# Kernel tuning notes

Hardware: AMD Instinct MI355X
Metric: run time of the kernel (lower is better)

## Reference

```python
import jax, jax.numpy as jnp
import numpy as np

EPS = 1e-4
RMS_EPS = 1e-5

def _rms_norm(x, w):
    # RMSNorm over last dim
    var = jnp.mean(x * x, axis=-1, keepdims=True)
    return x * jax.lax.rsqrt(var + RMS_EPS) * w


def setup_inputs() -> dict:
    key = jax.random.key(0)
    ks = jax.random.split(key, 6)
    T, d, h = 8192, 2048, 8192
    x = jax.random.normal(ks[0], (T, d), dtype=jnp.float32)
    Wq = jax.random.normal(ks[1], (d, d), dtype=jnp.float32) * 0.02
    Wk = jax.random.normal(ks[2], (d, d), dtype=jnp.float32) * 0.02
    fc1 = jax.random.normal(ks[3], (d, 2 * h), dtype=jnp.float32) * 0.02
    fc2 = jax.random.normal(ks[4], (h, d), dtype=jnp.float32) * 0.02
    norm_w = jnp.ones((d,), dtype=jnp.float32)
    cu_seqlens = (jnp.arange(9, dtype=jnp.int32) * (T // 8))  # 8 sequences of 1024
    return {"x": x, "Wq": Wq, "Wk": Wk, "fc1": fc1, "fc2": fc2,
            "norm_w": norm_w, "cu_seqlens": cu_seqlens}


def reference(x, Wq, Wk, fc1, fc2, norm_w, cu_seqlens):
    T, d = x.shape
    # sequence-start mask from jagged offsets
    seq_start = jnp.zeros((T,), dtype=bool).at[cu_seqlens[:-1]].set(True)

    # ---- RoutingModule: boundary prob p_t = clamp((1 - cos(q_{t-1}, k_t)) / 2) ----
    q = x @ Wq
    k = x @ Wk
    qn = q / jnp.linalg.norm(q, axis=-1, keepdims=True)
    kn = k / jnp.linalg.norm(k, axis=-1, keepdims=True)
    cos = jnp.sum(qn[:-1] * kn[1:], axis=-1)                    # [T-1]
    p = jnp.concatenate([jnp.ones((1,), x.dtype), (1.0 - cos) * 0.5])
    p = jnp.where(seq_start, 1.0, p)                            # first token of each seq is a boundary
    p = jnp.clip(p, EPS, 1.0 - EPS)
    b = p >= 0.5                                                # boundary indicator (STE fwd multiplier = 1)

    # ---- main network (tokenwise SwiGLU block w/ prenorm + residual);
    # tokenwise => computing on all tokens then gathering the boundary ones
    # equals computing on the selected (chunked) tokens ----
    xn = _rms_norm(x, norm_w)
    hh, g = jnp.split(xn @ fc1, 2, axis=-1)
    z = x + (jax.nn.silu(g) * hh) @ fc2                         # [T, d]

    # ---- DeChunk: inner2outer expansion. last_bd[t] = position of most recent
    # boundary <= t (b is True at seq starts, so it never crosses sequences) ----
    pos = jnp.where(b, jnp.arange(T), -1)
    last_bd = jax.lax.associative_scan(jnp.maximum, pos)        # [T]
    z_sel = z[last_bd]                                          # chunk rep broadcast to outer positions
    p_sel = p[last_bd]

    # ---- EMA selective scan over chunks, expressed on the outer axis:
    # h_t = a_t * h_{t-1} + b_t with a=1-p, b=p*z at boundaries; carry elsewhere;
    # reset (a=0) at sequence starts. Equivalent to mamba scan with A=-1,
    # dt=-log1p(-p), B=p, C=1 followed by index_select(cumsum(b)-1). ----
    a = jnp.where(seq_start, 0.0, jnp.where(b, 1.0 - p_sel, 1.0))[:, None]  # [T,1]
    bt = jnp.where(b[:, None], p_sel[:, None] * z_sel, 0.0)                  # [T,d]

    def comb(l, r):
        a1, b1 = l
        a2, b2 = r
        return a1 * a2, a2 * b1 + b2

    _, z_bar = jax.lax.associative_scan(comb, (a, bt))
    return z_bar
```

## Files before the change

### kernel.cpp

```cpp
#include <hip/hip_runtime.h>
#include <hip/hip_bf16.h>
#include <cstdint>
#include <cstddef>

typedef __bf16 bf16_t;
typedef bf16_t bf16x8 __attribute__((ext_vector_type(8)));
typedef _Float16 f16_t;
typedef f16_t f16x8 __attribute__((ext_vector_type(8)));
typedef float f32x4 __attribute__((ext_vector_type(4)));

#define EPS_P 1e-4
#define RMS_EPS_D 1e-5
#define WSCALE 64.0f

__device__ __forceinline__ void async_cp16(const void* g, void* l) {
  __builtin_amdgcn_global_load_lds(
      (const __attribute__((address_space(1))) unsigned int*)g,
      (__attribute__((address_space(3))) unsigned int*)l, 16, 0, 0);
}

#define SBAR() __builtin_amdgcn_s_barrier()
#define SCHED0() __builtin_amdgcn_sched_barrier(0)
#define LGKM0()                                        \
  do {                                                 \
    asm volatile("s_waitcnt lgkmcnt(0)" ::: "memory"); \
    __builtin_amdgcn_sched_barrier(0);                 \
  } while (0)
#define WAITV(N)                                           \
  do {                                                     \
    asm volatile("s_waitcnt vmcnt(" #N ")" ::: "memory");  \
    __builtin_amdgcn_sched_barrier(0);                     \
  } while (0)

__global__ __launch_bounds__(256) void transpose_cast(
    const float* __restrict__ in, bf16_t* __restrict__ out, int R, int C) {
  __shared__ float tile[32][33];
  int c0 = blockIdx.x * 32, r0 = blockIdx.y * 32;
  int tx = threadIdx.x & 31, ty = threadIdx.x >> 5;
#pragma unroll
  for (int s = 0; s < 4; ++s) {
    int r = ty + s * 8;
    tile[r][tx] = in[(size_t)(r0 + r) * C + c0 + tx];
  }
  __syncthreads();
#pragma unroll
  for (int s = 0; s < 4; ++s) {
    int cc = ty + s * 8;
    out[(size_t)(c0 + cc) * R + r0 + tx] = (bf16_t)tile[tx][cc];
  }
}

__global__ __launch_bounds__(256) void transpose_split(
    const float* __restrict__ in, f16_t* __restrict__ oh, f16_t* __restrict__ ol,
    int R, int C) {
  __shared__ float tile[32][33];
  int c0 = blockIdx.x * 32, r0 = blockIdx.y * 32;
  int tx = threadIdx.x & 31, ty = threadIdx.x >> 5;
#pragma unroll
  for (int s = 0; s < 4; ++s) {
    int r = ty + s * 8;
    tile[r][tx] = in[(size_t)(r0 + r) * C + c0 + tx];
  }
  __syncthreads();
#pragma unroll
  for (int s = 0; s < 4; ++s) {
    int cc = ty + s * 8;
    float v = tile[tx][cc] * WSCALE;
    f16_t hi = (f16_t)v;
    f16_t lo = (f16_t)(v - (float)hi);
    size_t idx = (size_t)(c0 + cc) * R + r0 + tx;
    oh[idx] = hi;
    ol[idx] = lo;
  }
}

__global__ __launch_bounds__(256) void split_x(
    const float* __restrict__ x, f16_t* __restrict__ xh, f16_t* __restrict__ xl,
    int n4) {
  int i = blockIdx.x * 256 + threadIdx.x;
  if (i >= n4) return;
  float4 v = *(const float4*)(x + (size_t)i * 4);
  f16_t h0 = (f16_t)v.x, h1 = (f16_t)v.y, h2 = (f16_t)v.z, h3 = (f16_t)v.w;
  f16_t hv[4] = {h0, h1, h2, h3};
  f16_t lv[4] = {(f16_t)(v.x - (float)h0), (f16_t)(v.y - (float)h1),
                 (f16_t)(v.z - (float)h2), (f16_t)(v.w - (float)h3)};
  *(short4*)(xh + (size_t)i * 4) = *(short4*)hv;
  *(short4*)(xl + (size_t)i * 4) = *(short4*)lv;
}

__global__ __launch_bounds__(256) void rmsnorm_cast(
    const float* __restrict__ X, const float* __restrict__ Wn,
    bf16_t* __restrict__ Xn, int d) {
  int row = blockIdx.x;
  const float* xr = X + (size_t)row * d;
  int t = threadIdx.x, l = t & 63, w = t >> 6;
  double ss = 0.0;
  for (int c = t * 4; c < d; c += 1024) {
    float4 v = *(const float4*)(xr + c);
    ss += (double)v.x * v.x + (double)v.y * v.y + (double)v.z * v.z + (double)v.w * v.w;
  }
#pragma unroll
  for (int o = 32; o > 0; o >>= 1) ss += __shfl_down(ss, o, 64);
  __shared__ double red[4];
  if (l == 0) red[w] = ss;
  __syncthreads();
  double tot = red[0] + red[1] + red[2] + red[3];
  float inv = (float)(1.0 / sqrt(tot / (double)d + RMS_EPS_D));
  for (int c = t * 4; c < d; c += 1024) {
    float4 v = *(const float4*)(xr + c);
    float4 wv = *(const float4*)(Wn + c);
    bf16_t* o = Xn + (size_t)row * d + c;
    o[0] = (bf16_t)(v.x * inv * wv.x);
    o[1] = (bf16_t)(v.y * inv * wv.y);
    o[2] = (bf16_t)(v.z * inv * wv.z);
    o[3] = (bf16_t)(v.w * inv * wv.w);
  }
}

__global__ __launch_bounds__(256) void gemm_f16_split(
    const f16_t* __restrict__ Ahg, const f16_t* __restrict__ Alg,
    const f16_t* __restrict__ Bhg, const f16_t* __restrict__ Blg,
    float* __restrict__ Out, int M, int N, int K, float outscale) {
  __shared__ f16_t Ah[128 * 32], Al[128 * 32], Bh[128 * 32], Bl[128 * 32];
  const int t = threadIdx.x, w = t >> 6, l = t & 63;
  const int m0 = blockIdx.y * 128, n0 = blockIdx.x * 128;
  const int wr = (w >> 1) * 64, wc = (w & 1) * 64;
  f32x4 acc[4][4] = {};
  const int ca0 = (w * 2) * 64 + l, ca1 = ca0 + 64;
  const int r0 = ca0 >> 2, ko0 = (ca0 & 3) * 8;
  const int r1 = ca1 >> 2, ko1 = (ca1 & 3) * 8;
  const int a_off = (wr + (l & 15)) * 32 + (l >> 4) * 8;
  const int b_off = (wc + (l & 15)) * 32 + (l >> 4) * 8;
  for (int k0 = 0; k0 < K; k0 += 32) {
    __syncthreads();
    async_cp16(Ahg + (size_t)(m0 + r0) * K + k0 + ko0, Ah + (w * 2 + 0) * 512);
    async_cp16(Ahg + (size_t)(m0 + r1) * K + k0 + ko1, Ah + (w * 2 + 1) * 512);
    async_cp16(Alg + (size_t)(m0 + r0) * K + k0 + ko0, Al + (w * 2 + 0) * 512);
    async_cp16(Alg + (size_t)(m0 + r1) * K + k0 + ko1, Al + (w * 2 + 1) * 512);
    async_cp16(Bhg + (size_t)(n0 + r0) * K + k0 + ko0, Bh + (w * 2 + 0) * 512);
    async_cp16(Bhg + (size_t)(n0 + r1) * K + k0 + ko1, Bh + (w * 2 + 1) * 512);
    async_cp16(Blg + (size_t)(n0 + r0) * K + k0 + ko0, Bl + (w * 2 + 0) * 512);
    async_cp16(Blg + (size_t)(n0 + r1) * K + k0 + ko1, Bl + (w * 2 + 1) * 512);
    __syncthreads();
    f16x8 ah[4], al[4], bh[4], bl[4];
#pragma unroll
    for (int i = 0; i < 4; ++i) {
      ah[i] = *(const f16x8*)(Ah + a_off + i * 512);
      al[i] = *(const f16x8*)(Al + a_off + i * 512);
    }
#pragma unroll
    for (int j = 0; j < 4; ++j) {
      bh[j] = *(const f16x8*)(Bh + b_off + j * 512);
      bl[j] = *(const f16x8*)(Bl + b_off + j * 512);
    }
#pragma unroll
    for (int i = 0; i < 4; ++i)
#pragma unroll
      for (int j = 0; j < 4; ++j) {
        acc[i][j] = __builtin_amdgcn_mfma_f32_16x16x32_f16(ah[i], bh[j], acc[i][j], 0, 0, 0);
        acc[i][j] = __builtin_amdgcn_mfma_f32_16x16x32_f16(ah[i], bl[j], acc[i][j], 0, 0, 0);
        acc[i][j] = __builtin_amdgcn_mfma_f32_16x16x32_f16(al[i], bh[j], acc[i][j], 0, 0, 0);
      }
  }
  const int col_l = l & 15, row_q = (l >> 4) * 4;
#pragma unroll
  for (int i = 0; i < 4; ++i)
#pragma unroll
    for (int j = 0; j < 4; ++j) {
      int col = n0 + wc + j * 16 + col_l;
#pragma unroll
      for (int r = 0; r < 4; ++r) {
        int row = m0 + wr + i * 16 + row_q + r;
        Out[(size_t)row * N + col] = acc[i][j][r] * outscale;
      }
    }
}

__global__ __launch_bounds__(256) void cos_p(
    const float* __restrict__ QK,
    const int* __restrict__ cu, int ncu,
    float* __restrict__ P, float* __restrict__ Aarr, float* __restrict__ Bf,
    int d) {
  int tk = blockIdx.x;
  int t = threadIdx.x, l = t & 63, w = t >> 6;
  __shared__ double rqk[4], rqq[4], rkk[4];
  double s_qk = 0, s_qq = 0, s_kk = 0;
  if (tk > 0) {
    const float* qr = QK + (size_t)(tk - 1) * (2 * d);
    const float* kr = QK + (size_t)tk * (2 * d) + d;
    for (int c = t * 4; c < d; c += 1024) {
      float4 qv = *(const float4*)(qr + c);
      float4 kv = *(const float4*)(kr + c);
      s_qk += (double)qv.x * kv.x + (double)qv.y * kv.y + (double)qv.z * kv.z + (double)qv.w * kv.w;
      s_qq += (double)qv.x * qv.x + (double)qv.y * qv.y + (double)qv.z * qv.z + (double)qv.w * qv.w;
      s_kk += (double)kv.x * kv.x + (double)kv.y * kv.y + (double)kv.z * kv.z + (double)kv.w * kv.w;
    }
#pragma unroll
    for (int o = 32; o > 0; o >>= 1) {
      s_qk += __shfl_down(s_qk, o, 64);
      s_qq += __shfl_down(s_qq, o, 64);
      s_kk += __shfl_down(s_kk, o, 64);
    }
    if (l == 0) { rqk[w] = s_qk; rqq[w] = s_qq; rkk[w] = s_kk; }
    __syncthreads();
  }
  if (t == 0) {
    bool start = false;
    for (int i = 0; i + 1 < ncu; ++i)
      if (cu[i] == tk) start = true;
    double p;
    if (tk == 0) {
      p = 1.0;
    } else {
      double dqk = rqk[0] + rqk[1] + rqk[2] + rqk[3];
      double dqq = rqq[0] + rqq[1] + rqq[2] + rqq[3];
      double dkk = rkk[0] + rkk[1] + rkk[2] + rkk[3];
      double cosv = dqk / sqrt(dqq * dkk);
      p = (1.0 - cosv) * 0.5;
    }
    if (start) p = 1.0;
    if (p < EPS_P) p = EPS_P;
    if (p > 1.0 - EPS_P) p = 1.0 - EPS_P;
    float b = (p >= 0.5) ? 1.0f : 0.0f;
    float a = start ? 0.0f : ((b > 0.5f) ? (float)(1.0 - p) : 1.0f);
    P[tk] = (float)p; Aarr[tk] = a; Bf[tk] = b;
  }
}

__global__ void pfx_kernel(const float* __restrict__ Aarr, float* __restrict__ Pfx,
                           float* __restrict__ Ac, int T) {
  int c = threadIdx.x;
  if (c * 64 < T) {
    float Pv = 1.0f;
    for (int i = 0; i < 64; ++i) {
      int tt = c * 64 + i;
      Pv *= Aarr[tt];
      Pfx[tt] = Pv;
    }
    Ac[c] = Pv;
  }
}

template <bool SWIGLU>
__global__ __launch_bounds__(512, 2) void gemm256(
    const bf16_t* __restrict__ A, const bf16_t* __restrict__ B,
    const float* __restrict__ X, float* __restrict__ Outf,
    bf16_t* __restrict__ Outb, int M, int N, int K, int H) {
  __shared__ char lds[2][2][32768];
  const int t = threadIdx.x;
  const int l = t & 63, w = t >> 6;
  const int wm = w >> 1, wn = w & 1;
  const int m0 = blockIdx.y * 256;
  const int NT = K >> 6;
  const size_t sB = (size_t)K * 2;
  const int nb = blockIdx.x * (SWIGLU ? 128 : 256);
  const char* Ab = (const char*)A + (size_t)m0 * sB;
  const char* Bb0 = (const char*)B + (size_t)nb * sB;
  const char* Bb1 = (const char*)B + (size_t)(SWIGLU ? (H + nb) : (nb + 128)) * sB;
  const int srow = l >> 3;
  const size_t laneoff = (size_t)srow * sB + (size_t)(((l & 7) ^ srow) << 4);
  const int fr_row = (l & 15) << 7;
  const int g0 = (((l >> 4) ^ (l & 7)) << 4);
  const int g1 = ((((l >> 4) + 4) ^ (l & 7)) << 4);
  f32x4 acc[2][4][4] = {};

  auto STAGE = [&](const char* src, char* ldsb) {
    const char* s = src + (size_t)(w << 4) * sB + laneoff;
    async_cp16(s, ldsb + (w << 11));
    async_cp16(s + 8 * sB, ldsb + (w << 11) + 1024);
  };

  STAGE(Ab, lds[0][0]);
  STAGE(Ab + 128 * sB, lds[0][0] + 16384);
  STAGE(Bb0, lds[0][1]);
  STAGE(Bb1, lds[0][1] + 16384);
  STAGE(Ab + 128, lds[1][0]);
  STAGE(Ab + 128 * sB + 128, lds[1][0] + 16384);
  STAGE(Bb0 + 128, lds[1][1]);
  WAITV(6);
  SBAR();

  for (int kt = 0; kt < NT; ++kt) {
    const int buf = kt & 1;
    char* Als = lds[buf][0];
    char* Bls = lds[buf][1];
    const char* Abl = Als + ((wm << 6) << 7) + fr_row;
    const char* Bbl = Bls + ((wn << 6) << 7) + fr_row;
    bf16x8 a0[4], a1[4], bfr[4];

#pragma unroll
    for (int i = 0; i < 4; ++i) {
      a0[i] = *(const bf16x8*)(Abl + i * 2048 + g0);
      a1[i] = *(const bf16x8*)(Abl + i * 2048 + g1);
    }
#pragma unroll
    for (int j = 0; j < 4; ++j) bfr[j] = *(const bf16x8*)(Bbl + j * 2048 + g0);
    if (kt + 1 < NT) STAGE(Bb1 + (size_t)(kt + 1) * 128, lds[buf ^ 1][1] + 16384);
    SBAR();
    LGKM0();
    __builtin_amdgcn_s_setprio(1);
#pragma unroll
    for (int i = 0; i < 4; ++i)
#pragma unroll
      for (int j = 0; j < 4; ++j)
        acc[0][i][j] = __builtin_amdgcn_mfma_f32_16x16x32_bf16(a0[i], bfr[j], acc[0][i][j], 0, 0, 0);
    __builtin_amdgcn_s_setprio(0);
    SCHED0();
    SBAR();

#pragma unroll
    for (int j = 0; j < 4; ++j) bfr[j] = *(const bf16x8*)(Bbl + j * 2048 + g1);
    if (kt + 2 < NT) STAGE(Ab + (size_t)(kt + 2) * 128, Als);
    SBAR();
    LGKM0();
    __builtin_amdgcn_s_setprio(1);
#pragma unroll
    for (int i = 0; i < 4; ++i)
#pragma unroll
      for (int j = 0; j < 4; ++j)
        acc[0][i][j] = __builtin_amdgcn_mfma_f32_16x16x32_bf16(a1[i], bfr[j], acc[0][i][j], 0, 0, 0);
    __builtin_amdgcn_s_setprio(0);
    SCHED0();
    SBAR();

#pragma unroll
    for (int j = 0; j < 4; ++j) bfr[j] = *(const bf16x8*)(Bbl + 16384 + j * 2048 + g0);
    if (kt + 2 < NT) {
      STAGE(Ab + 128 * sB + (size_t)(kt + 2) * 128, Als + 16384);
      STAGE(Bb0 + (size_t)(kt + 2) * 128, Bls);
    }
    SBAR();
    LGKM0();
    __builtin_amdgcn_s_setprio(1);
#pragma unroll
    for (int i = 0; i < 4; ++i)
#pragma unroll
      for (int j = 0; j < 4; ++j)
        acc[1][i][j] = __builtin_amdgcn_mfma_f32_16x16x32_bf16(a0[i], bfr[j], acc[1][i][j], 0, 0, 0);
    __builtin_amdgcn_s_setprio(0);
    SCHED0();
    SBAR();

#pragma unroll
    for (int j = 0; j < 4; ++j) bfr[j] = *(const bf16x8*)(Bbl + 16384 + j * 2048 + g1);
    SBAR();
    LGKM0();
    __builtin_amdgcn_s_setprio(1);
#pragma unroll
    for (int i = 0; i < 4; ++i)
#pragma unroll
      for (int j = 0; j < 4; ++j)
        acc[1][i][j] = __builtin_amdgcn_mfma_f32_16x16x32_bf16(a1[i], bfr[j], acc[1][i][j], 0, 0, 0);
    __builtin_amdgcn_s_setprio(0);
    SCHED0();
    if (kt + 1 < NT) {
      if (kt + 2 < NT) WAITV(6);
      else WAITV(0);
    }
    SBAR();
  }

  const int col_l = l & 15, row_q = (l >> 4) * 4;
  if (SWIGLU) {
    const int ucol0 = nb + (wn << 6);
#pragma unroll
    for (int i = 0; i < 4; ++i)
#pragma unroll
      for (int j = 0; j < 4; ++j) {
        const int col = ucol0 + j * 16 + col_l;
        const int row = m0 + (wm << 6) + i * 16 + row_q;
#pragma unroll
        for (int r = 0; r < 4; ++r) {
          float hh = acc[0][i][j][r];
          float g = acc[1][i][j][r];
          float s = g / (1.0f + expf(-g));
          Outb[(size_t)(row + r) * N + col] = (bf16_t)(s * hh);
        }
      }
  } else {
#pragma unroll
    for (int p = 0; p < 2; ++p)
#pragma unroll
      for (int i = 0; i < 4; ++i)
#pragma unroll
        for (int j = 0; j < 4; ++j) {
          const int col = nb + p * 128 + (wn << 6) + j * 16 + col_l;
          const int row = m0 + (wm << 6) + i * 16 + row_q;
#pragma unroll
          for (int r = 0; r < 4; ++r) {
            size_t idx = (size_t)(row + r) * N + col;
            Outf[idx] = X[idx] + acc[p][i][j][r];
          }
        }
  }
}

__global__ __launch_bounds__(256) void scan1(
    float* __restrict__ Z, const float* __restrict__ P,
    const float* __restrict__ Aarr, const float* __restrict__ Bf, int d) {
  int c = blockIdx.x;
  int col = blockIdx.y * 512 + threadIdx.x * 2;
  __shared__ float sa[64], sp[64], sb[64];
  if (threadIdx.x < 64) {
    int tt = c * 64 + threadIdx.x;
    sa[threadIdx.x] = Aarr[tt];
    sp[threadIdx.x] = P[tt];
    sb[threadIdx.x] = Bf[tt];
  }
  __syncthreads();
  float hx = 0.0f, hy = 0.0f;
  for (int i = 0; i < 64; ++i) {
    int row = c * 64 + i;
    float a = sa[i];
    float2* zp = (float2*)(Z + (size_t)row * d + col);
    if (sb[i] > 0.5f) {
      float2 zv = *zp;
      float pp = sp[i];
      hx = a * hx + pp * zv.x;
      hy = a * hy + pp * zv.y;
    } else {
      hx = a * hx;
      hy = a * hy;
    }
    float2 hv; hv.x = hx; hv.y = hy;
    *zp = hv;
  }
}

__global__ __launch_bounds__(256) void scan2(
    const float* __restrict__ Z, const float* __restrict__ Ac,
    float* __restrict__ Hprev, int d, int NC) {
  int col = blockIdx.x * 256 + threadIdx.x;
  float H = 0.0f;
  for (int c = 0; c < NC; ++c) {
    Hprev[(size_t)c * d + col] = H;
    float E = Z[(size_t)(c * 64 + 63) * d + col];
    H = Ac[c] * H + E;
  }
}

__global__ __launch_bounds__(256) void scan3(
    float* __restrict__ Z, const float* __restrict__ Pfx,
    const float* __restrict__ Hprev, int d) {
  int row = blockIdx.x;
  int c = row >> 6;
  float pf = Pfx[row];
  int col = threadIdx.x * 8;
  const float* hp = Hprev + (size_t)c * d + col;
  float4 h0 = *(const float4*)hp;
  float4 h1 = *(const float4*)(hp + 4);
  float* zp = Z + (size_t)row * d + col;
  float4 z0 = *(const float4*)zp;
  float4 z1 = *(const float4*)(zp + 4);
  z0.x += pf * h0.x; z0.y += pf * h0.y; z0.z += pf * h0.z; z0.w += pf * h0.w;
  z1.x += pf * h1.x; z1.y += pf * h1.y; z1.z += pf * h1.z; z1.w += pf * h1.w;
  *(float4*)zp = z0;
  *(float4*)(zp + 4) = z1;
}

extern "C" void kernel_launch(void* const* d_in, const int* in_sizes, int n_in,
                              void* d_out, int out_size, void* d_ws, size_t ws_size,
                              hipStream_t stream) {
  const float* x   = (const float*)d_in[0];
  const float* Wq  = (const float*)d_in[1];
  const float* Wk  = (const float*)d_in[2];
  const float* fc1 = (const float*)d_in[3];
  const float* fc2 = (const float*)d_in[4];
  const float* nw  = (const float*)d_in[5];
  const int*   cu  = (const int*)d_in[6];
  const int ncu = in_sizes[6];
  const int d = in_sizes[5];
  const int T = in_sizes[0] / d;
  const int h = in_sizes[4] / d;
  const int NC = T / 64;
  float* zout = (float*)d_out;

  char* ws = (char*)d_ws;
  size_t off = 0;
  auto alloc = [&](size_t bytes) -> void* {
    void* p = ws + off;
    off += (bytes + 255) & ~(size_t)255;
    return p;
  };
  float*  qk   = (float*)alloc((size_t)T * 2 * d * 4);
  bf16_t* u    = (bf16_t*)qk;
  bf16_t* xn   = (bf16_t*)alloc((size_t)T * d * 2);
  size_t szXh = (size_t)T * d * 2;
  size_t szWt = (size_t)2 * d * d * 2;
  char* regionA = (char*)alloc(2 * szXh + 2 * szWt);
  f16_t* Xh  = (f16_t*)regionA;
  f16_t* Xl  = (f16_t*)(regionA + szXh);
  f16_t* Wth = (f16_t*)(regionA + 2 * szXh);
  f16_t* Wtl = (f16_t*)(regionA + 2 * szXh + szWt);
  bf16_t* fc1t = (bf16_t*)regionA;
  bf16_t* fc2t = (bf16_t*)(regionA + (size_t)2 * h * d * 2);
  float*  P    = (float*)alloc((size_t)T * 4);
  float*  Aa   = (float*)alloc((size_t)T * 4);
  float*  Bf   = (float*)alloc((size_t)T * 4);
  float*  Pfx  = (float*)alloc((size_t)T * 4);
  float*  Ac   = (float*)alloc((size_t)NC * 4);
  float*  Hprev= (float*)alloc((size_t)NC * d * 4);

  split_x<<<dim3(T * d / 1024), 256, 0, stream>>>(x, Xh, Xl, T * d / 4);
  transpose_split<<<dim3(d / 32, d / 32), 256, 0, stream>>>(Wq, Wth, Wtl, d, d);
  transpose_split<<<dim3(d / 32, d / 32), 256, 0, stream>>>(
      Wk, Wth + (size_t)d * d, Wtl + (size_t)d * d, d, d);
  gemm_f16_split<<<dim3(2 * d / 128, T / 128), 256, 0, stream>>>(
      Xh, Xl, Wth, Wtl, qk, T, 2 * d, d, 1.0f / WSCALE);
  cos_p<<<dim3(T), 256, 0, stream>>>(qk, cu, ncu, P, Aa, Bf, d);
  pfx_kernel<<<dim3(1), 128, 0, stream>>>(Aa, Pfx, Ac, T);

  transpose_cast<<<dim3(2 * h / 32, d / 32), 256, 0, stream>>>(fc1, fc1t, d, 2 * h);
  transpose_cast<<<dim3(d / 32, h / 32), 256, 0, stream>>>(fc2, fc2t, h, d);
  rmsnorm_cast<<<dim3(T), 256, 0, stream>>>(x, nw, xn, d);
  gemm256<true><<<dim3(h / 128, T / 256), 512, 0, stream>>>(
      xn, fc1t, nullptr, nullptr, u, T, h, d, h);
  gemm256<false><<<dim3(d / 256, T / 256), 512, 0, stream>>>(
      u, fc2t, x, zout, nullptr, T, d, h, 0);
  scan1<<<dim3(NC, d / 512), 256, 0, stream>>>(zout, P, Aa, Bf, d);
  scan2<<<dim3(d / 256), 256, 0, stream>>>(zout, Ac, Hprev, d, NC);
  scan3<<<dim3(T), 256, 0, stream>>>(zout, Pfx, Hprev, d);
}
```

Baseline: 1.593 ms.

## Software-pipeline LDS fragment reads and remap GEMM workgroups across XCDs

The bf16 GEMM loop is restructured so LDS fragment reads for the next sub-step are issued before the current MFMA block, and the explicit lgkmcnt(0) waits are removed. This lets LDS latency overlap with matrix math. The launch grid is also flattened to 1D, and block IDs are remapped so that consecutive tiles land on the same XCD (blockIdx mod 8 chunking), which is meant to improve L2 reuse. Correctness now depends on the compiler inserting the right LDS waits and on the retuned vmcnt counts and barrier placement.

```diff
diff --git a/kernel.cpp b/kernel.cpp
--- a/kernel.cpp
+++ b/kernel.cpp
@@ -21,11 +21,6 @@
 
 #define SBAR() __builtin_amdgcn_s_barrier()
 #define SCHED0() __builtin_amdgcn_sched_barrier(0)
-#define LGKM0()                                        \
-  do {                                                 \
-    asm volatile("s_waitcnt lgkmcnt(0)" ::: "memory"); \
-    __builtin_amdgcn_sched_barrier(0);                 \
-  } while (0)
 #define WAITV(N)                                           \
   do {                                                     \
     asm volatile("s_waitcnt vmcnt(" #N ")" ::: "memory");  \
@@ -245,119 +240,126 @@
 __global__ __launch_bounds__(512, 2) void gemm256(
     const bf16_t* __restrict__ A, const bf16_t* __restrict__ B,
     const float* __restrict__ X, float* __restrict__ Outf,
-    bf16_t* __restrict__ Outb, int M, int N, int K, int H) {
+    bf16_t* __restrict__ Outb, int M, int N, int K, int H, int gx) {
   __shared__ char lds[2][2][32768];
   const int t = threadIdx.x;
   const int l = t & 63, w = t >> 6;
   const int wm = w >> 1, wn = w & 1;
-  const int m0 = blockIdx.y * 256;
+  const int cpx = (int)gridDim.x >> 3;
+  const int bid = (int)blockIdx.x;
+  const int wgid = (bid & 7) * cpx + (bid >> 3);
+  const int bx = wgid % gx, by = wgid / gx;
+  const int m0 = by * 256;
   const int NT = K >> 6;
   const size_t sB = (size_t)K * 2;
-  const int nb = blockIdx.x * (SWIGLU ? 128 : 256);
+  const int nb = bx * (SWIGLU ? 128 : 256);
   const char* Ab = (const char*)A + (size_t)m0 * sB;
   const char* Bb0 = (const char*)B + (size_t)nb * sB;
   const char* Bb1 = (const char*)B + (size_t)(SWIGLU ? (H + nb) : (nb + 128)) * sB;
   const int srow = l >> 3;
   const size_t laneoff = (size_t)srow * sB + (size_t)(((l & 7) ^ srow) << 4);
+  const size_t F = (size_t)(w << 4) * sB + laneoff;
+  const size_t s8 = 8 * sB;
+  const char* rA0 = Ab + F;
+  const char* rA1 = Ab + (size_t)128 * sB + F;
+  const char* rB0 = Bb0 + F;
+  const char* rB1 = Bb1 + F;
   const int fr_row = (l & 15) << 7;
-  const int g0 = (((l >> 4) ^ (l & 7)) << 4);
-  const int g1 = ((((l >> 4) + 4) ^ (l & 7)) << 4);
+  const int gk0 = (((l >> 4) ^ (l & 7)) << 4);
+  const int gk1 = ((((l >> 4) + 4) ^ (l & 7)) << 4);
+  const int wmoff = (wm << 13) + fr_row;
+  const int wnoff = (wn << 13) + fr_row;
   f32x4 acc[2][4][4] = {};
-
-  auto STAGE = [&](const char* src, char* ldsb) {
-    const char* s = src + (size_t)(w << 4) * sB + laneoff;
-    async_cp16(s, ldsb + (w << 11));
-    async_cp16(s + 8 * sB, ldsb + (w << 11) + 1024);
+  bf16x8 a0[4], a1[4], bX[4], bY[4];
+
+  auto ST = [&](const char* s, char* d) {
+    async_cp16(s, d);
+    async_cp16(s + s8, d + 1024);
   };
-
-  STAGE(Ab, lds[0][0]);
-  STAGE(Ab + 128 * sB, lds[0][0] + 16384);
-  STAGE(Bb0, lds[0][1]);
-  STAGE(Bb1, lds[0][1] + 16384);
-  STAGE(Ab + 128, lds[1][0]);
-  STAGE(Ab + 128 * sB + 128, lds[1][0] + 16384);
-  STAGE(Bb0 + 128, lds[1][1]);
-  WAITV(6);
-  SBAR();
+  auto RD = [&](bf16x8 (&dst)[4], const char* base, int g) {
+#pragma unroll
+    for (int j = 0; j < 4; ++j) dst[j] = *(const bf16x8*)(base + j * 2048 + g);
+  };
+  auto MM = [&](f32x4 (&C)[4][4], bf16x8 (&Af)[4], bf16x8 (&Bfr)[4]) {
+#pragma unroll
+    for (int i = 0; i < 4; ++i)
+#pragma unroll
+      for (int j = 0; j < 4; ++j)
+        C[i][j] = __builtin_amdgcn_mfma_f32_16x16x32_bf16(Af[i], Bfr[j], C[i][j], 0, 0, 0);
+  };
+
+  {
+    char* dA0 = lds[0][0] + (w << 11);
+    char* dB0 = lds[0][1] + (w << 11);
+    char* dA1 = lds[1][0] + (w << 11);
+    char* dB1 = lds[1][1] + (w << 11);
+    ST(rA0, dA0); ST(rA1, dA0 + 16384);
+    ST(rB0, dB0); ST(rB1, dB0 + 16384);
+    ST(rA0 + 128, dA1); ST(rA1 + 128, dA1 + 16384);
+    ST(rB0 + 128, dB1);
+    WAITV(8);
+    SBAR();
+    SCHED0();
+    RD(a0, lds[0][0] + wmoff, gk0);
+    RD(bX, lds[0][1] + wnoff, gk0);
+  }
 
   for (int kt = 0; kt < NT; ++kt) {
-    const int buf = kt & 1;
-    char* Als = lds[buf][0];
-    char* Bls = lds[buf][1];
-    const char* Abl = Als + ((wm << 6) << 7) + fr_row;
-    const char* Bbl = Bls + ((wn << 6) << 7) + fr_row;
-    bf16x8 a0[4], a1[4], bfr[4];
-
-#pragma unroll
-    for (int i = 0; i < 4; ++i) {
-      a0[i] = *(const bf16x8*)(Abl + i * 2048 + g0);
-      a1[i] = *(const bf16x8*)(Abl + i * 2048 + g1);
-    }
-#pragma unroll
-    for (int j = 0; j < 4; ++j) bfr[j] = *(const bf16x8*)(Bbl + j * 2048 + g0);
-    if (kt + 1 < NT) STAGE(Bb1 + (size_t)(kt + 1) * 128, lds[buf ^ 1][1] + 16384);
+    const int b = kt & 1;
+    const char* Abl = lds[b][0] + wmoff;
+    const char* Bbl = lds[b][1] + wnoff;
+    char* dAc = lds[b][0] + (w << 11);
+    char* dBc = lds[b][1] + (w << 11);
+    char* dBn = lds[b ^ 1][1] + (w << 11);
+    const size_t ko = (size_t)kt * 128;
+
+    RD(a1, Abl, gk1);
+    RD(bY, Bbl, gk1);
+    if (kt + 1 < NT) ST(rB1 + ko + 128, dBn + 16384);
+    SCHED0();
+    __builtin_amdgcn_s_setprio(1);
+    MM(acc[0], a0, bX);
+    __builtin_amdgcn_s_setprio(0);
+    SCHED0();
+    if (kt + 1 < NT) { WAITV(8); } else { WAITV(0); }
     SBAR();
-    LGKM0();
+    SCHED0();
+
+    RD(bX, Bbl + 16384, gk0);
+    SCHED0();
     __builtin_amdgcn_s_setprio(1);
-#pragma unroll
-    for (int i = 0; i < 4; ++i)
-#pragma unroll
-      for (int j = 0; j < 4; ++j)
-        acc[0][i][j] = __builtin_amdgcn_mfma_f32_16x16x32_bf16(a0[i], bfr[j], acc[0][i][j], 0, 0, 0);
+    MM(acc[0], a1, bY);
     __builtin_amdgcn_s_setprio(0);
     SCHED0();
     SBAR();
-
-#pragma unroll
-    for (int j = 0; j < 4; ++j) bfr[j] = *(const bf16x8*)(Bbl + j * 2048 + g1);
-    if (kt + 2 < NT) STAGE(Ab + (size_t)(kt + 2) * 128, Als);
+    SCHED0();
+
+    RD(bY, Bbl + 16384, gk1);
+    if (kt + 2 < NT) ST(rA0 + ko + 256, dAc);
+    SCHED0();
+    __builtin_amdgcn_s_setprio(1);
+    MM(acc[1], a0, bX);
+    __builtin_amdgcn_s_setprio(0);
+    SCHED0();
+    if (kt + 2 < NT) { WAITV(4); } else { WAITV(0); }
     SBAR();
-    LGKM0();
+    SCHED0();
+
+    if (kt + 1 < NT) {
+      RD(a0, lds[b ^ 1][0] + wmoff, gk0);
+      RD(bX, lds[b ^ 1][1] + wnoff, gk0);
+    }
+    if (kt + 2 < NT) {
+      ST(rA1 + ko + 256, dAc + 16384);
+      ST(rB0 + ko + 256, dBc);
+    }
+    SCHED0();
     __builtin_amdgcn_s_setprio(1);
-#pragma unroll
-    for (int i = 0; i < 4; ++i)
-#pragma unroll
-      for (int j = 0; j < 4; ++j)
-        acc[0][i][j] = __builtin_amdgcn_mfma_f32_16x16x32_bf16(a1[i], bfr[j], acc[0][i][j], 0, 0, 0);
+    MM(acc[1], a1, bY);
     __builtin_amdgcn_s_setprio(0);
     SCHED0();
     SBAR();
-
-#pragma unroll
-    for (int j = 0; j < 4; ++j) bfr[j] = *(const bf16x8*)(Bbl + 16384 + j * 2048 + g0);
-    if (kt + 2 < NT) {
-      STAGE(Ab + 128 * sB + (size_t)(kt + 2) * 128, Als + 16384);
-      STAGE(Bb0 + (size_t)(kt + 2) * 128, Bls);
-    }
-    SBAR();
-    LGKM0();
-    __builtin_amdgcn_s_setprio(1);
-#pragma unroll
-    for (int i = 0; i < 4; ++i)
-#pragma unroll
-      for (int j = 0; j < 4; ++j)
-        acc[1][i][j] = __builtin_amdgcn_mfma_f32_16x16x32_bf16(a0[i], bfr[j], acc[1][i][j], 0, 0, 0);
-    __builtin_amdgcn_s_setprio(0);
-    SCHED0();
-    SBAR();
-
-#pragma unroll
-    for (int j = 0; j < 4; ++j) bfr[j] = *(const bf16x8*)(Bbl + 16384 + j * 2048 + g1);
-    SBAR();
-    LGKM0();
-    __builtin_amdgcn_s_setprio(1);
-#pragma unroll
-    for (int i = 0; i < 4; ++i)
-#pragma unroll
-      for (int j = 0; j < 4; ++j)
-        acc[1][i][j] = __builtin_amdgcn_mfma_f32_16x16x32_bf16(a1[i], bfr[j], acc[1][i][j], 0, 0, 0);
-    __builtin_amdgcn_s_setprio(0);
-    SCHED0();
-    if (kt + 1 < NT) {
-      if (kt + 2 < NT) WAITV(6);
-      else WAITV(0);
-    }
-    SBAR();
+    SCHED0();
   }
 
   const int col_l = l & 15, row_q = (l >> 4) * 4;
@@ -513,10 +515,10 @@
   transpose_cast<<<dim3(2 * h / 32, d / 32), 256, 0, stream>>>(fc1, fc1t, d, 2 * h);
   transpose_cast<<<dim3(d / 32, h / 32), 256, 0, stream>>>(fc2, fc2t, h, d);
   rmsnorm_cast<<<dim3(T), 256, 0, stream>>>(x, nw, xn, d);
-  gemm256<true><<<dim3(h / 128, T / 256), 512, 0, stream>>>(
-      xn, fc1t, nullptr, nullptr, u, T, h, d, h);
-  gemm256<false><<<dim3(d / 256, T / 256), 512, 0, stream>>>(
-      u, fc2t, x, zout, nullptr, T, d, h, 0);
+  gemm256<true><<<dim3((h / 128) * (T / 256)), 512, 0, stream>>>(
+      xn, fc1t, nullptr, nullptr, u, T, h, d, h, h / 128);
+  gemm256<false><<<dim3((d / 256) * (T / 256)), 512, 0, stream>>>(
+      u, fc2t, x, zout, nullptr, T, d, h, 0, d / 256);
   scan1<<<dim3(NC, d / 512), 256, 0, stream>>>(zout, P, Aa, Bf, d);
   scan2<<<dim3(d / 256), 256, 0, stream>>>(zout, Ac, Hprev, d, NC);
   scan3<<<dim3(T), 256, 0, stream>>>(zout, Pfx, Hprev, d);
```

Result: faster. 1.512 ms (-5.1%).
